# Optimization experiments

Hardware: AMD Instinct MI355X
Metric: run time of the kernel (lower is better)

## Reference

```python
import jax, jax.numpy as jnp
import numpy as np

N, E, IN_DIM, HID, OUT = 50000, 800000, 128, 128, 64


def setup_inputs() -> dict:
    key = jax.random.key(0)
    k = jax.random.split(key, 6)
    h = jax.random.normal(k[0], (N, IN_DIM), dtype=jnp.float32)
    edge_index = jax.random.randint(k[1], (2, E), 0, N, dtype=jnp.int64)
    s_in, s_hid = 1.0 / np.sqrt(IN_DIM), 1.0 / np.sqrt(HID)
    W_gcn = jax.random.uniform(k[2], (IN_DIM, HID), jnp.float32, -s_in, s_in)
    b_gcn = jnp.zeros((HID,), jnp.float32)
    W_fc = jax.random.uniform(k[3], (HID, OUT), jnp.float32, -s_hid, s_hid)
    b_fc = jax.random.uniform(k[4], (OUT,), jnp.float32, -s_hid, s_hid)
    return {"h": h, "edge_index": edge_index, "W_gcn": W_gcn,
            "b_gcn": b_gcn, "W_fc": W_fc, "b_fc": b_fc}


def reference(h, edge_index, W_gcn, b_gcn, W_fc, b_fc):
    n = h.shape[0]
    # GCNConv: transform, add self-loops, symmetric normalization, scatter-add
    x = h @ W_gcn                                   # [N, HID]
    loop = jnp.arange(n, dtype=edge_index.dtype)
    row = jnp.concatenate([edge_index[0], loop])    # source nodes
    col = jnp.concatenate([edge_index[1], loop])    # destination nodes
    deg = jax.ops.segment_sum(jnp.ones_like(col, dtype=x.dtype), col,
                              num_segments=n)       # in-degree incl. self-loop
    dinv = jnp.where(deg > 0, jax.lax.rsqrt(deg), 0.0)
    norm = dinv[row] * dinv[col]                    # [E+N]
    msg = x[row] * norm[:, None]                    # gather + scale
    agg = jax.ops.segment_sum(msg, col, num_segments=n) + b_gcn
    # ReLU then projection
    return jax.nn.relu(agg) @ W_fc + b_fc
```

## Files before the change

### kernel.cpp

```cpp
#include <hip/hip_runtime.h>

#define N_NODES 50000
#define N_EDGES 800000
#define NBKT 196
#define BCAP 6144

typedef __attribute__((ext_vector_type(4))) float floatx4;
typedef __attribute__((ext_vector_type(8))) _Float16 half8;
typedef __attribute__((ext_vector_type(2))) _Float16 half2v;

#define O_PTR   0UL
#define O_GF    200192UL
#define O_DINV  201472UL
#define O_ESRC  401664UL
#define O_W1    3801856UL
#define O_W2    3834624UL
#define O_STG   3851008UL
#define O_H16   16651008UL

__global__ __launch_bounds__(256) void k_binA(const int* __restrict__ ei,
                                              int* __restrict__ gfill,
                                              unsigned* __restrict__ staging) {
    __shared__ int cnt[NBKT];
    __shared__ int gbase[NBKT];
    __shared__ int s_i64;
    int t = threadIdx.x;
    if (t < 64) {
        unsigned w = ((const unsigned*)ei)[2 * t + 1];
        unsigned long long m = __ballot(w == 0u);
        if (t == 0) s_i64 = (__popcll(m) >= 60) ? 1 : 0;
    }
    for (int i = t; i < NBKT; i += 256) cnt[i] = 0;
    __syncthreads();
    bool i64 = s_i64 != 0;
    int e0 = blockIdx.x * 4096 + t * 16;
    int sv[16], dvv[16];
    if (i64) {
        const int4* ps = (const int4*)(ei) + (e0 >> 1);
        const int4* pd = (const int4*)(ei + 2 * (size_t)N_EDGES) + (e0 >> 1);
#pragma unroll
        for (int g = 0; g < 8; ++g) {
            if (e0 + 2 * g < N_EDGES) {
                int4 s4 = ps[g], d4 = pd[g];
                sv[2 * g] = s4.x; sv[2 * g + 1] = s4.z;
                dvv[2 * g] = d4.x; dvv[2 * g + 1] = d4.z;
            } else { dvv[2 * g] = -1; dvv[2 * g + 1] = -1; }
        }
    } else {
        const int4* ps = (const int4*)(ei) + (e0 >> 2);
        const int4* pd = (const int4*)(ei + (size_t)N_EDGES) + (e0 >> 2);
#pragma unroll
        for (int g = 0; g < 4; ++g) {
            if (e0 + 4 * g < N_EDGES) {
                int4 s4 = ps[g], d4 = pd[g];
                sv[4 * g] = s4.x; sv[4 * g + 1] = s4.y; sv[4 * g + 2] = s4.z; sv[4 * g + 3] = s4.w;
                dvv[4 * g] = d4.x; dvv[4 * g + 1] = d4.y; dvv[4 * g + 2] = d4.z; dvv[4 * g + 3] = d4.w;
            } else { dvv[4 * g] = -1; dvv[4 * g + 1] = -1; dvv[4 * g + 2] = -1; dvv[4 * g + 3] = -1; }
        }
    }
    unsigned pk[16]; int rk[16]; short bk[16];
#pragma unroll
    for (int j = 0; j < 16; ++j) {
        int d = dvv[j];
        if (d >= 0 && e0 + j < N_EDGES) {
            int b = d >> 8;
            bk[j] = (short)b;
            pk[j] = (unsigned)sv[j] | ((unsigned)(d & 255) << 16);
            rk[j] = atomicAdd(&cnt[b], 1);
        } else bk[j] = -1;
    }
    __syncthreads();
    for (int i = t; i < NBKT; i += 256)
        gbase[i] = atomicAdd(&gfill[i], cnt[i]);
    __syncthreads();
#pragma unroll
    for (int j = 0; j < 16; ++j) {
        if (bk[j] >= 0) {
            int pos = gbase[bk[j]] + rk[j];
            if (pos < BCAP) staging[(size_t)bk[j] * BCAP + pos] = pk[j];
        }
    }
}

__global__ __launch_bounds__(256) void k_binB(const unsigned* __restrict__ staging,
                                              const int* __restrict__ gfill,
                                              const float* __restrict__ h,
                                              const float* __restrict__ Wg,
                                              const float* __restrict__ Wf,
                                              int* __restrict__ ptr,
                                              float* __restrict__ dinv,
                                              _Float16* __restrict__ h16,
                                              _Float16* __restrict__ W1,
                                              _Float16* __restrict__ W2,
                                              int* __restrict__ esrc) {
    __shared__ unsigned se[BCAP];
    __shared__ int lcnt[256];
    __shared__ int lscan[256];
    __shared__ int cur[256];
    __shared__ float sdinv[256];
    __shared__ int s_cb;
    int b = blockIdx.x, t = threadIdx.x;
    if (b < 64) {
        int i = b * 256 + t;
        int n = i >> 7, k = i & 127;
        W1[i] = (_Float16)Wg[k * 128 + n];
    } else if (b < 96) {
        int i = (b - 64) * 256 + t;
        int n = i >> 7, k = i & 127;
        W2[i] = (_Float16)Wf[k * 64 + n];
    }
    int nbase = b * 256;
    int nn = min(256, N_NODES - nbase);
    int cnt = min(gfill[b], BCAP);
    if (t < 64) {
        int acc = 0;
        for (int i = t; i < b; i += 64) acc += min(gfill[i], BCAP);
#pragma unroll
        for (int off = 32; off > 0; off >>= 1) acc += __shfl_down(acc, off);
        if (t == 0) s_cb = acc;
    }
    lcnt[t] = 0;
    __syncthreads();
    int cb = s_cb;
    const unsigned* st = staging + (size_t)b * BCAP;
    for (int i = t; i < cnt; i += 256) {
        unsigned p = st[i];
        se[i] = p;
        atomicAdd(&lcnt[p >> 16], 1);
    }
    __syncthreads();
    int v = lcnt[t];
    lscan[t] = v;
    __syncthreads();
    for (int off = 1; off < 256; off <<= 1) {
        int x = (t >= off) ? lscan[t - off] : 0;
        __syncthreads(); lscan[t] += x; __syncthreads();
    }
    int segstart = cb + (lscan[t] - v);
    float dv = rsqrtf((float)(v + 1));
    if (t < nn) {
        int node = nbase + t;
        ptr[node] = segstart;
        dinv[node] = dv;
        sdinv[t] = dv;
        cur[t] = segstart;
    }
    __syncthreads();
    for (int i = t; i < cnt; i += 256) {
        unsigned p = se[i];
        int pos = atomicAdd(&cur[p >> 16], 1);
        esrc[pos] = (int)(p & 0xffffu);
    }
    int half = t >> 7;
    int col = t & 127;
    for (int r = half; r < nn; r += 2) {
        int node = nbase + r;
        h16[(size_t)node * 128 + col] = (_Float16)(h[(size_t)node * 128 + col] * sdinv[r]);
    }
}

__global__ __launch_bounds__(256) void k_aggF(const _Float16* __restrict__ h16,
                                              const int* __restrict__ ptr,
                                              const int* __restrict__ esrc,
                                              const float* __restrict__ dinv,
                                              const _Float16* __restrict__ W1,
                                              const _Float16* __restrict__ W2,
                                              const float* __restrict__ bg,
                                              const float* __restrict__ bfc,
                                              float* __restrict__ out) {
    __shared__ _Float16 ut[16 * 128];
    __shared__ _Float16 z[16 * 128];
    int wave = threadIdx.x >> 6;
    int lane = threadIdx.x & 63;
    int nb = blockIdx.x * 16;
    for (int q = 0; q < 4; ++q) {
        int node = nb + wave * 4 + q;
        int p0 = ptr[node];
        int p1 = (node + 1 < N_NODES) ? ptr[node + 1] : N_EDGES;
        half2v us = *(const half2v*)(h16 + (size_t)node * 128 + lane * 2);
        float a0 = (float)us[0], a1 = (float)us[1];
        for (int base = p0; base < p1; base += 64) {
            int cnt = p1 - base; if (cnt > 64) cnt = 64;
            int idx = 0;
            if (lane < cnt) idx = esrc[base + lane];
            int j = 0;
            for (; j + 8 <= cnt; j += 8) {
                int s0 = __shfl(idx, j),     s1 = __shfl(idx, j + 1);
                int s2 = __shfl(idx, j + 2), s3 = __shfl(idx, j + 3);
                int s4 = __shfl(idx, j + 4), s5 = __shfl(idx, j + 5);
                int s6 = __shfl(idx, j + 6), s7 = __shfl(idx, j + 7);
                half2v u0 = *(const half2v*)(h16 + (size_t)s0 * 128 + lane * 2);
                half2v u1 = *(const half2v*)(h16 + (size_t)s1 * 128 + lane * 2);
                half2v u2 = *(const half2v*)(h16 + (size_t)s2 * 128 + lane * 2);
                half2v u3 = *(const half2v*)(h16 + (size_t)s3 * 128 + lane * 2);
                half2v u4 = *(const half2v*)(h16 + (size_t)s4 * 128 + lane * 2);
                half2v u5 = *(const half2v*)(h16 + (size_t)s5 * 128 + lane * 2);
                half2v u6 = *(const half2v*)(h16 + (size_t)s6 * 128 + lane * 2);
                half2v u7 = *(const half2v*)(h16 + (size_t)s7 * 128 + lane * 2);
                a0 += (float)u0[0] + (float)u1[0] + (float)u2[0] + (float)u3[0]
                    + (float)u4[0] + (float)u5[0] + (float)u6[0] + (float)u7[0];
                a1 += (float)u0[1] + (float)u1[1] + (float)u2[1] + (float)u3[1]
                    + (float)u4[1] + (float)u5[1] + (float)u6[1] + (float)u7[1];
            }
            for (; j + 4 <= cnt; j += 4) {
                int s0 = __shfl(idx, j),     s1 = __shfl(idx, j + 1);
                int s2 = __shfl(idx, j + 2), s3 = __shfl(idx, j + 3);
                half2v u0 = *(const half2v*)(h16 + (size_t)s0 * 128 + lane * 2);
                half2v u1 = *(const half2v*)(h16 + (size_t)s1 * 128 + lane * 2);
                half2v u2 = *(const half2v*)(h16 + (size_t)s2 * 128 + lane * 2);
                half2v u3 = *(const half2v*)(h16 + (size_t)s3 * 128 + lane * 2);
                a0 += (float)u0[0] + (float)u1[0] + (float)u2[0] + (float)u3[0];
                a1 += (float)u0[1] + (float)u1[1] + (float)u2[1] + (float)u3[1];
            }
            for (; j < cnt; ++j) {
                int s = __shfl(idx, j);
                half2v uu = *(const half2v*)(h16 + (size_t)s * 128 + lane * 2);
                a0 += (float)uu[0]; a1 += (float)uu[1];
            }
        }
        float sc = dinv[node];
        int r = wave * 4 + q;
        ut[r * 128 + lane * 2]     = (_Float16)(a0 * sc);
        ut[r * 128 + lane * 2 + 1] = (_Float16)(a1 * sc);
    }
    __syncthreads();
    int quad = lane >> 4, l15 = lane & 15;
    half8 a[4];
#pragma unroll
    for (int kk = 0; kk < 4; ++kk)
        a[kk] = *(const half8*)(ut + l15 * 128 + kk * 32 + quad * 8);
#pragma unroll
    for (int tt = 0; tt < 2; ++tt) {
        floatx4 acc = {0.f, 0.f, 0.f, 0.f};
        int n = (wave * 2 + tt) * 16 + l15;
#pragma unroll
        for (int kk = 0; kk < 4; ++kk) {
            half8 bb = *(const half8*)(W1 + n * 128 + kk * 32 + quad * 8);
            acc = __builtin_amdgcn_mfma_f32_16x16x32_f16(a[kk], bb, acc, 0, 0, 0);
        }
        float bias = bg[n];
#pragma unroll
        for (int i = 0; i < 4; ++i)
            z[(quad * 4 + i) * 128 + n] = (_Float16)fmaxf(acc[i] + bias, 0.f);
    }
    __syncthreads();
    half8 a2[4];
#pragma unroll
    for (int kk = 0; kk < 4; ++kk)
        a2[kk] = *(const half8*)(z + l15 * 128 + kk * 32 + quad * 8);
    {
        floatx4 acc = {0.f, 0.f, 0.f, 0.f};
        int n = wave * 16 + l15;
#pragma unroll
        for (int kk = 0; kk < 4; ++kk) {
            half8 bb = *(const half8*)(W2 + n * 128 + kk * 32 + quad * 8);
            acc = __builtin_amdgcn_mfma_f32_16x16x32_f16(a2[kk], bb, acc, 0, 0, 0);
        }
        float bias = bfc[n];
#pragma unroll
        for (int i = 0; i < 4; ++i)
            out[(size_t)(nb + quad * 4 + i) * 64 + n] = acc[i] + bias;
    }
}

extern "C" void kernel_launch(void* const* d_in, const int* in_sizes, int n_in,
                              void* d_out, int out_size, void* d_ws, size_t ws_size,
                              hipStream_t stream) {
    (void)in_sizes; (void)n_in; (void)out_size; (void)ws_size;
    const float* h  = (const float*)d_in[0];
    const int*   ei = (const int*)d_in[1];
    const float* Wg = (const float*)d_in[2];
    const float* bg = (const float*)d_in[3];
    const float* Wf = (const float*)d_in[4];
    const float* bf = (const float*)d_in[5];
    float* out = (float*)d_out;

    char* ws = (char*)d_ws;
    int*      ptr   = (int*)(ws + O_PTR);
    int*      gfill = (int*)(ws + O_GF);
    float*    dinv  = (float*)(ws + O_DINV);
    int*      esrc  = (int*)(ws + O_ESRC);
    _Float16* W1    = (_Float16*)(ws + O_W1);
    _Float16* W2    = (_Float16*)(ws + O_W2);
    unsigned* staging = (unsigned*)(ws + O_STG);
    _Float16* h16   = (_Float16*)(ws + O_H16);

    hipMemsetAsync(gfill, 0, NBKT * sizeof(int), stream);
    k_binA<<<NBKT, 256, 0, stream>>>(ei, gfill, staging);
    k_binB<<<NBKT, 256, 0, stream>>>(staging, gfill, h, Wg, Wf,
                                     ptr, dinv, h16, W1, W2, esrc);
    k_aggF<<<N_NODES / 16, 256, 0, stream>>>(h16, ptr, esrc, dinv,
                                             W1, W2, bg, bf, out);
}
```

Measured before the change: 155.1 us.

## Pad CSR segments to multiples of four and gather four neighbor rows per wave with 16-byte loads

```diff
diff --git a/kernel.cpp b/kernel.cpp
--- a/kernel.cpp
+++ b/kernel.cpp
@@ -4,18 +4,19 @@
 #define N_EDGES 800000
 #define NBKT 196
 #define BCAP 6144
+#define ZROW 50000
+#define UTS 136
 
 typedef __attribute__((ext_vector_type(4))) float floatx4;
 typedef __attribute__((ext_vector_type(8))) _Float16 half8;
-typedef __attribute__((ext_vector_type(2))) _Float16 half2v;
 
 #define O_PTR   0UL
 #define O_GF    200192UL
 #define O_DINV  201472UL
 #define O_ESRC  401664UL
-#define O_W1    3801856UL
-#define O_W2    3834624UL
-#define O_STG   3851008UL
+#define O_W1    4204032UL
+#define O_W2    4236800UL
+#define O_STG   4253184UL
 #define O_H16   16651008UL
 
 __global__ __launch_bounds__(256) void k_binA(const int* __restrict__ ei,
@@ -108,6 +109,8 @@
         int i = (b - 64) * 256 + t;
         int n = i >> 7, k = i & 127;
         W2[i] = (_Float16)Wf[k * 64 + n];
+    } else if (b == 96 && t < 128) {
+        h16[(size_t)ZROW * 128 + t] = (_Float16)0.f;
     }
     int nbase = b * 256;
     int nn = min(256, N_NODES - nbase);
@@ -117,7 +120,7 @@
         for (int i = t; i < b; i += 64) acc += min(gfill[i], BCAP);
 #pragma unroll
         for (int off = 32; off > 0; off >>= 1) acc += __shfl_down(acc, off);
-        if (t == 0) s_cb = acc;
+        if (t == 0) s_cb = acc + b * 768;
     }
     lcnt[t] = 0;
     __syncthreads();
@@ -130,20 +133,22 @@
     }
     __syncthreads();
     int v = lcnt[t];
-    lscan[t] = v;
+    int pv = (v + 3) & ~3;
+    lscan[t] = pv;
     __syncthreads();
     for (int off = 1; off < 256; off <<= 1) {
         int x = (t >= off) ? lscan[t - off] : 0;
         __syncthreads(); lscan[t] += x; __syncthreads();
     }
-    int segstart = cb + (lscan[t] - v);
+    int segstart = cb + (lscan[t] - pv);
     float dv = rsqrtf((float)(v + 1));
     if (t < nn) {
         int node = nbase + t;
-        ptr[node] = segstart;
+        ptr[node] = (segstart << 11) | (pv >> 2);
         dinv[node] = dv;
         sdinv[t] = dv;
         cur[t] = segstart;
+        for (int i = v; i < pv; ++i) esrc[segstart + i] = ZROW;
     }
     __syncthreads();
     for (int i = t; i < cnt; i += 256) {
@@ -168,67 +173,67 @@
                                               const float* __restrict__ bg,
                                               const float* __restrict__ bfc,
                                               float* __restrict__ out) {
-    __shared__ _Float16 ut[16 * 128];
-    __shared__ _Float16 z[16 * 128];
+    __shared__ _Float16 ut[16 * UTS];
+    __shared__ _Float16 z[16 * UTS];
     int wave = threadIdx.x >> 6;
     int lane = threadIdx.x & 63;
     int nb = blockIdx.x * 16;
+    int lane4 = lane >> 4;
+    int colo = (lane & 15) * 8;
     for (int q = 0; q < 4; ++q) {
         int node = nb + wave * 4 + q;
-        int p0 = ptr[node];
-        int p1 = (node + 1 < N_NODES) ? ptr[node + 1] : N_EDGES;
-        half2v us = *(const half2v*)(h16 + (size_t)node * 128 + lane * 2);
-        float a0 = (float)us[0], a1 = (float)us[1];
-        for (int base = p0; base < p1; base += 64) {
-            int cnt = p1 - base; if (cnt > 64) cnt = 64;
+        int word = ptr[node];
+        int base = word >> 11;
+        int ngr = word & 0x7ff;
+        float acc[8];
+        if (lane4 == 0) {
+            half8 us = *(const half8*)(h16 + (size_t)node * 128 + colo);
+#pragma unroll
+            for (int j = 0; j < 8; ++j) acc[j] = (float)us[j];
+        } else {
+#pragma unroll
+            for (int j = 0; j < 8; ++j) acc[j] = 0.f;
+        }
+        for (int w = 0; w < ngr; w += 16) {
+            int gmax = ngr - w; if (gmax > 16) gmax = 16;
             int idx = 0;
-            if (lane < cnt) idx = esrc[base + lane];
-            int j = 0;
-            for (; j + 8 <= cnt; j += 8) {
-                int s0 = __shfl(idx, j),     s1 = __shfl(idx, j + 1);
-                int s2 = __shfl(idx, j + 2), s3 = __shfl(idx, j + 3);
-                int s4 = __shfl(idx, j + 4), s5 = __shfl(idx, j + 5);
-                int s6 = __shfl(idx, j + 6), s7 = __shfl(idx, j + 7);
-                half2v u0 = *(const half2v*)(h16 + (size_t)s0 * 128 + lane * 2);
-                half2v u1 = *(const half2v*)(h16 + (size_t)s1 * 128 + lane * 2);
-                half2v u2 = *(const half2v*)(h16 + (size_t)s2 * 128 + lane * 2);
-                half2v u3 = *(const half2v*)(h16 + (size_t)s3 * 128 + lane * 2);
-                half2v u4 = *(const half2v*)(h16 + (size_t)s4 * 128 + lane * 2);
-                half2v u5 = *(const half2v*)(h16 + (size_t)s5 * 128 + lane * 2);
-                half2v u6 = *(const half2v*)(h16 + (size_t)s6 * 128 + lane * 2);
-                half2v u7 = *(const half2v*)(h16 + (size_t)s7 * 128 + lane * 2);
-                a0 += (float)u0[0] + (float)u1[0] + (float)u2[0] + (float)u3[0]
-                    + (float)u4[0] + (float)u5[0] + (float)u6[0] + (float)u7[0];
-                a1 += (float)u0[1] + (float)u1[1] + (float)u2[1] + (float)u3[1]
-                    + (float)u4[1] + (float)u5[1] + (float)u6[1] + (float)u7[1];
+            if (lane < gmax * 4) idx = esrc[base + w * 4 + lane];
+            if (gmax == 16) {
+#pragma unroll
+                for (int g = 0; g < 16; ++g) {
+                    int row = __shfl(idx, g * 4 + lane4);
+                    half8 u = *(const half8*)(h16 + (size_t)row * 128 + colo);
+#pragma unroll
+                    for (int j = 0; j < 8; ++j) acc[j] += (float)u[j];
+                }
+            } else {
+                for (int g = 0; g < gmax; ++g) {
+                    int row = __shfl(idx, g * 4 + lane4);
+                    half8 u = *(const half8*)(h16 + (size_t)row * 128 + colo);
+#pragma unroll
+                    for (int j = 0; j < 8; ++j) acc[j] += (float)u[j];
+                }
             }
-            for (; j + 4 <= cnt; j += 4) {
-                int s0 = __shfl(idx, j),     s1 = __shfl(idx, j + 1);
-                int s2 = __shfl(idx, j + 2), s3 = __shfl(idx, j + 3);
-                half2v u0 = *(const half2v*)(h16 + (size_t)s0 * 128 + lane * 2);
-                half2v u1 = *(const half2v*)(h16 + (size_t)s1 * 128 + lane * 2);
-                half2v u2 = *(const half2v*)(h16 + (size_t)s2 * 128 + lane * 2);
-                half2v u3 = *(const half2v*)(h16 + (size_t)s3 * 128 + lane * 2);
-                a0 += (float)u0[0] + (float)u1[0] + (float)u2[0] + (float)u3[0];
-                a1 += (float)u0[1] + (float)u1[1] + (float)u2[1] + (float)u3[1];
-            }
-            for (; j < cnt; ++j) {
-                int s = __shfl(idx, j);
-                half2v uu = *(const half2v*)(h16 + (size_t)s * 128 + lane * 2);
-                a0 += (float)uu[0]; a1 += (float)uu[1];
-            }
-        }
-        float sc = dinv[node];
-        int r = wave * 4 + q;
-        ut[r * 128 + lane * 2]     = (_Float16)(a0 * sc);
-        ut[r * 128 + lane * 2 + 1] = (_Float16)(a1 * sc);
+        }
+#pragma unroll
+        for (int j = 0; j < 8; ++j) {
+            acc[j] += __shfl_xor(acc[j], 16);
+            acc[j] += __shfl_xor(acc[j], 32);
+        }
+        if (lane < 16) {
+            float sc = dinv[node];
+            half8 o;
+#pragma unroll
+            for (int j = 0; j < 8; ++j) o[j] = (_Float16)(acc[j] * sc);
+            *(half8*)(ut + (wave * 4 + q) * UTS + colo) = o;
+        }
     }
     __syncthreads();
     int quad = lane >> 4, l15 = lane & 15;
     half8 a[4];
 #pragma unroll
     for (int kk = 0; kk < 4; ++kk)
-        a[kk] = *(const half8*)(ut + l15 * 128 + kk * 32 + quad * 8);
+        a[kk] = *(const half8*)(ut + l15 * UTS + kk * 32 + quad * 8);
 #pragma unroll
     for (int tt = 0; tt < 2; ++tt) {
         floatx4 acc = {0.f, 0.f, 0.f, 0.f};
@@ -241,13 +246,13 @@
         float bias = bg[n];
 #pragma unroll
         for (int i = 0; i < 4; ++i)
-            z[(quad * 4 + i) * 128 + n] = (_Float16)fmaxf(acc[i] + bias, 0.f);
+            z[(quad * 4 + i) * UTS + n] = (_Float16)fmaxf(acc[i] + bias, 0.f);
     }
     __syncthreads();
     half8 a2[4];
 #pragma unroll
     for (int kk = 0; kk < 4; ++kk)
-        a2[kk] = *(const half8*)(z + l15 * 128 + kk * 32 + quad * 8);
+        a2[kk] = *(const half8*)(z + l15 * UTS + kk * 32 + quad * 8);
     {
         floatx4 acc = {0.f, 0.f, 0.f, 0.f};
         int n = wave * 16 + l15;
```

Result: slower. 194.5 us (+25.4%).
